# Kernel tuning notes

Hardware: AMD Instinct MI355X
Metric: run time of the kernel (lower is better)

Reference implementation:

```python
import jax, jax.numpy as jnp
import numpy as np

B, S, D, H = 2, 2048, 1024, 16
DH = D // H  # 64


def setup_inputs() -> dict:
    key = jax.random.key(0)
    ks = jax.random.split(key, 9)
    scale = 0.02
    x = jax.random.normal(ks[0], (B, S, D), dtype=jnp.float32)
    # per-head QKV weights stacked over heads: [H, D, DH]
    Wq = jax.random.normal(ks[1], (H, D, DH), dtype=jnp.float32) * scale
    Wk = jax.random.normal(ks[2], (H, D, DH), dtype=jnp.float32) * scale
    Wv = jax.random.normal(ks[3], (H, D, DH), dtype=jnp.float32) * scale
    bq = jax.random.normal(ks[4], (H, DH), dtype=jnp.float32) * scale
    bk = jax.random.normal(ks[5], (H, DH), dtype=jnp.float32) * scale
    bv = jax.random.normal(ks[6], (H, DH), dtype=jnp.float32) * scale
    Wo = jax.random.normal(ks[7], (D, D), dtype=jnp.float32) * scale
    bo = jax.random.normal(ks[8], (D,), dtype=jnp.float32) * scale
    return {"x": x, "Wq": Wq, "bq": bq, "Wk": Wk, "bk": bk, "Wv": Wv, "bv": bv, "Wo": Wo, "bo": bo}


def reference(x, Wq, bq, Wk, bk, Wv, bv, Wo, bo):
    # per-head projections: [B, H, S, DH]
    q = jnp.einsum('bsd,hde->bhse', x, Wq) + bq[None, :, None, :]
    k = jnp.einsum('bsd,hde->bhse', x, Wk) + bk[None, :, None, :]
    v = jnp.einsum('bsd,hde->bhse', x, Wv) + bv[None, :, None, :]
    scores = jnp.einsum('bhse,bhte->bhst', q, k) / jnp.sqrt(jnp.float32(DH))
    probs = jax.nn.softmax(scores, axis=-1)  # [B, H, S, S]
    ctx = jnp.einsum('bhst,bhte->bhse', probs, v)  # [B, H, S, DH]
    # concat heads: [B, S, H*DH]
    ctx = jnp.transpose(ctx, (0, 2, 1, 3)).reshape(x.shape[0], x.shape[1], H * DH)
    out = ctx @ Wo + bo  # output projection; dropout p=0 -> identity
    return out
```

## Files before the change

kernel.cpp:

```cpp
#include <hip/hip_runtime.h>

typedef __attribute__((ext_vector_type(8))) short short8;
typedef __attribute__((ext_vector_type(4))) float f32x4;
typedef __attribute__((ext_vector_type(16))) float f32x16;
typedef __attribute__((ext_vector_type(4))) unsigned short us4;
typedef unsigned short ushort;

typedef __attribute__((address_space(3))) void lds_void;
typedef __attribute__((address_space(1))) void gbl_void;

__device__ __forceinline__ ushort f2bf(float f) {
  unsigned u = __float_as_uint(f);
  u += 0x7fff + ((u >> 16) & 1);
  return (ushort)(u >> 16);
}

__global__ void cvt_x_kernel(const float* __restrict__ x, ushort* __restrict__ xb) {
  int i = (blockIdx.x * 256 + threadIdx.x) * 8;
  float4 a = *(const float4*)(x + i);
  float4 b = *(const float4*)(x + i + 4);
  ushort o[8];
  o[0] = f2bf(a.x); o[1] = f2bf(a.y); o[2] = f2bf(a.z); o[3] = f2bf(a.w);
  o[4] = f2bf(b.x); o[5] = f2bf(b.y); o[6] = f2bf(b.z); o[7] = f2bf(b.w);
  *(short8*)(xb + i) = *(short8*)o;
}

__global__ void wprep_kernel(const float* __restrict__ Wq, const float* __restrict__ Wk,
                             const float* __restrict__ Wv, const float* __restrict__ Wo,
                             ushort* __restrict__ wqkv_t, ushort* __restrict__ wo_t) {
  __shared__ float T[64][65];
  const int k0 = blockIdx.x * 64;
  const int hy = blockIdx.y;
  const int m = blockIdx.z;
  const float* src = (m == 0) ? Wq : (m == 1) ? Wk : (m == 2) ? Wv : Wo;
#pragma unroll
  for (int it = 0; it < 16; ++it) {
    int idx = it * 256 + threadIdx.x;
    int kk = idx >> 6, e = idx & 63;
    float v = (m < 3) ? src[hy * 65536 + (k0 + kk) * 64 + e]
                      : src[(k0 + kk) * 1024 + hy * 64 + e];
    T[e][kk] = v;
  }
  __syncthreads();
  ushort* dst = (m < 3) ? (wqkv_t + (size_t)(m * 1024 + hy * 64) * 1024)
                        : (wo_t + (size_t)(hy * 64) * 1024);
#pragma unroll
  for (int it = 0; it < 2; ++it) {
    int c = it * 256 + threadIdx.x;
    int e = c >> 3, kc = (c & 7) * 8;
    ushort o[8];
#pragma unroll
    for (int j = 0; j < 8; ++j) o[j] = f2bf(T[e][kc + j]);
    *(short8*)&dst[(size_t)e * 1024 + k0 + kc] = *(short8*)o;
  }
}

__global__ __launch_bounds__(512, 2) void gemm_qkv256(
    const ushort* __restrict__ A, const ushort* __restrict__ Bt,
    const float* __restrict__ b0, const float* __restrict__ b1, const float* __restrict__ b2,
    ushort* __restrict__ qfp, ushort* __restrict__ kfp, ushort* __restrict__ vfp) {
  __shared__ ushort sm[3][2][256][32];
  const int tid = threadIdx.x;
  const int lane = tid & 63;
  const int wave = tid >> 6;
  const int l15 = lane & 15, l4 = lane >> 4;
  const int wwr = wave >> 2, wc = wave & 3;
  const int p0 = blockIdx.x;
  const int p = (p0 & 7) * 24 + (p0 >> 3);
  const int by = p & 15, bx = p >> 4;
  const int row0 = by * 256, col0 = bx * 256;

  const ushort* Ag = A + (size_t)row0 * 1024;
  const ushort* Bg = Bt + (size_t)col0 * 1024;
  char* smb = (char*)&sm[0][0][0][0];

  auto stage = [&](int buf, int kt, int c0) {
    const int c = c0 + tid;
    const int row = (c & 1023) >> 2;
    const int slot = c & 3;
    const int scol = (slot ^ ((row >> 1) & 3)) * 8;
    const ushort* src = ((c >> 10) ? Bg : Ag) + (size_t)row * 1024 + kt * 32 + scol;
    __builtin_amdgcn_global_load_lds((const gbl_void*)src,
        (lds_void*)(smb + buf * 32768 + (c0 + (tid & ~63)) * 16), 16, 0, 0);
  };
  auto rdA = [&](int buf, int mfg) {
    const int row = wwr * 128 + mfg * 16 + l15;
    return *(const short8*)(smb + buf * 32768 + row * 64 + ((l4 ^ ((row >> 1) & 3)) << 4));
  };
  auto rdB = [&](int buf, int nf) {
    const int row = wc * 64 + nf * 16 + l15;
    return *(const short8*)(smb + buf * 32768 + 16384 + row * 64 + ((l4 ^ ((row >> 1) & 3)) << 4));
  };

  f32x4 acc[8][4];
#pragma unroll
  for (int i = 0; i < 8; ++i)
#pragma unroll
    for (int j = 0; j < 4; ++j) acc[i][j] = (f32x4){0.f, 0.f, 0.f, 0.f};

  stage(0, 0, 0); stage(0, 0, 512); stage(0, 0, 1024); stage(0, 0, 1536);
  stage(1, 1, 0); stage(1, 1, 512); stage(1, 1, 1024); stage(1, 1, 1536);

  int buf = 0;
  for (int kt = 0; kt < 32; ++kt) {
    if (kt == 31) asm volatile("s_waitcnt vmcnt(0)" ::: "memory");
    else          asm volatile("s_waitcnt vmcnt(4)" ::: "memory");
    asm volatile("s_barrier" ::: "memory");
    const int kn = kt + 2;
    const int bn = (buf >= 1) ? buf - 1 : buf + 2;
    short8 bfr[4], af[4];
#pragma unroll
    for (int nf = 0; nf < 4; ++nf) bfr[nf] = rdB(buf, nf);
#pragma unroll
    for (int mf = 0; mf < 4; ++mf) af[mf] = rdA(buf, mf);
    if (kn < 32) { stage(bn, kn, 0); stage(bn, kn, 512); }
    __builtin_amdgcn_s_setprio(1);
#pragma unroll
    for (int mf = 0; mf < 4; ++mf)
#pragma unroll
      for (int nf = 0; nf < 4; ++nf)
        acc[mf][nf] = __builtin_amdgcn_mfma_f32_16x16x32_bf16(af[mf], bfr[nf], acc[mf][nf], 0, 0, 0);
    __builtin_amdgcn_s_setprio(0);
    asm volatile("s_barrier" ::: "memory");
#pragma unroll
    for (int mf = 0; mf < 4; ++mf) af[mf] = rdA(buf, 4 + mf);
    if (kn < 32) { stage(bn, kn, 1024); stage(bn, kn, 1536); }
    __builtin_amdgcn_s_setprio(1);
#pragma unroll
    for (int mf = 0; mf < 4; ++mf)
#pragma unroll
      for (int nf = 0; nf < 4; ++nf)
        acc[4 + mf][nf] = __builtin_amdgcn_mfma_f32_16x16x32_bf16(af[mf], bfr[nf], acc[4 + mf][nf], 0, 0, 0);
    __builtin_amdgcn_s_setprio(0);
    buf = (buf == 2) ? 0 : buf + 1;
  }

  const float QSCALE = 0.18033688f;
#pragma unroll
  for (int mfg = 0; mfg < 8; ++mfg) {
    const int row = row0 + wwr * 128 + mfg * 16 + l4 * 4;
    const int bb = row >> 11, s = row & 2047;
#pragma unroll
    for (int nf = 0; nf < 4; ++nf) {
      const int col = col0 + wc * 64 + nf * 16 + l15;
      if (col < 2048) {
        const int cf = col & 1023;
        const int h = cf >> 6, d = cf & 63;
        const int bh = bb * 16 + h;
        ushort* dst = (col < 1024) ? qfp : kfp;
        const float bias = ((col < 1024) ? b0 : b1)[cf];
        const float sc = (col < 1024) ? QSCALE : 1.0f;
        const size_t base =
            ((((size_t)bh * 64 + (s >> 5)) * 4 + (d >> 4)) * 64 + ((d >> 3) & 1) * 32 + (s & 31)) * 8 +
            (d & 7);
#pragma unroll
        for (int r = 0; r < 4; ++r) dst[base + r * 8] = f2bf((acc[mfg][nf][r] + bias) * sc);
      } else {
        const int ef = col - 2048;
        const int h = ef >> 6, e = ef & 63;
        const int bh = bb * 16 + h;
        const float bias = b2[ef];
        ushort o4[4];
#pragma unroll
        for (int r = 0; r < 4; ++r) o4[r] = f2bf(acc[mfg][nf][r] + bias);
        const size_t addr =
            ((((size_t)bh * 2 + (e >> 5)) * 128 + (s >> 4)) * 64 + ((s >> 3) & 1) * 32 + (e & 31)) * 8 +
            (s & 7);
        *(us4*)&vfp[addr] = *(us4*)o4;
      }
    }
  }
}

__global__ __launch_bounds__(256) void gemm_out_kernel(
    const ushort* __restrict__ A, const ushort* __restrict__ Bt,
    const float* __restrict__ b0, float* __restrict__ C) {
  __shared__ ushort lA[128 * 32];
  __shared__ ushort lB[128 * 32];
  const int tid = threadIdx.x;
  const int lane = tid & 63;
  const int wave = tid >> 6;
  const int l15 = lane & 15, l4 = lane >> 4;
  const int wr = wave >> 1, wc = wave & 1;
  const int row0 = blockIdx.y * 128, col0 = blockIdx.x * 128;

  f32x4 acc[4][4];
#pragma unroll
  for (int i = 0; i < 4; ++i)
#pragma unroll
    for (int j = 0; j < 4; ++j) acc[i][j] = (f32x4){0.f, 0.f, 0.f, 0.f};

  const ushort* Ag = A + (size_t)row0 * 1024;
  const ushort* Bg = Bt + (size_t)col0 * 1024;

  for (int k0 = 0; k0 < 1024; k0 += 32) {
#pragma unroll
    for (int c = 0; c < 2; ++c) {
      const int chunk = tid + c * 256;
      const int rr = chunk >> 2;
      const int kc = (chunk & 3) * 8;
      const unsigned lbase = (unsigned)((tid & ~63) + c * 256) * 16;
      __builtin_amdgcn_global_load_lds((const gbl_void*)(Ag + (size_t)rr * 1024 + k0 + kc),
                                       (lds_void*)((char*)lA + lbase), 16, 0, 0);
      __builtin_amdgcn_global_load_lds((const gbl_void*)(Bg + (size_t)rr * 1024 + k0 + kc),
                                       (lds_void*)((char*)lB + lbase), 16, 0, 0);
    }
    __syncthreads();
    short8 af[4], bfr[4];
#pragma unroll
    for (int i = 0; i < 4; ++i)
      af[i] = *(const short8*)&lA[(wr * 64 + i * 16 + l15) * 32 + l4 * 8];
#pragma unroll
    for (int j = 0; j < 4; ++j)
      bfr[j] = *(const short8*)&lB[(wc * 64 + j * 16 + l15) * 32 + l4 * 8];
#pragma unroll
    for (int i = 0; i < 4; ++i)
#pragma unroll
      for (int j = 0; j < 4; ++j)
        acc[i][j] = __builtin_amdgcn_mfma_f32_16x16x32_bf16(af[i], bfr[j], acc[i][j], 0, 0, 0);
    __syncthreads();
  }

#pragma unroll
  for (int i = 0; i < 4; ++i) {
    const int row = row0 + wr * 64 + i * 16 + l4 * 4;
#pragma unroll
    for (int j = 0; j < 4; ++j) {
      const int col = col0 + wc * 64 + j * 16 + l15;
      const float bias = b0[col];
#pragma unroll
      for (int r = 0; r < 4; ++r)
        C[(size_t)(row + r) * 1024 + col] = acc[i][j][r] + bias;
    }
  }
}

__global__ __launch_bounds__(256, 2) void attn_kernel(const ushort* __restrict__ qf,
                                                      const ushort* __restrict__ kf,
                                                      const ushort* __restrict__ vf,
                                                      ushort* __restrict__ ctx) {
  __shared__ ushort sm[4][8192];
  const int tid = threadIdx.x;
  const int lane = tid & 63, wave = tid >> 6;
  const int l31 = lane & 31, hi = lane >> 5;
  const int p0 = blockIdx.x;
  const int idx = p0 >> 3;
  const int bh = (p0 & 7) * 4 + (idx >> 4);
  const int q0 = ((idx & 15) * 4 + wave) * 32;
  const int b = bh >> 4, h = bh & 15;

  const size_t bhbase = (size_t)bh * 131072;
  const ushort* qfb = qf + bhbase + (size_t)(q0 >> 5) * 2048 + (size_t)lane * 8;
  const ushort* kfbh = kf + bhbase;
  const ushort* vfbh = vf + bhbase;
  char* smb = (char*)&sm[0][0];

  short8 qb[4];
#pragma unroll
  for (int kk = 0; kk < 4; ++kk)
    qb[kk] = *(const short8*)(qfb + kk * 512);

  auto stage = [&](int buf, int t0) {
    const ushort* s0 = kfbh + (size_t)(t0 >> 5) * 2048 + tid * 8;
    const ushort* s1 = s0 + 2048;
    const ushort* s2 = vfbh + (size_t)(t0 >> 4) * 512 + tid * 8;
    const ushort* s3 = s2 + 65536;
    char* d = smb + buf * 16384 + (tid & ~63) * 16;
    __builtin_amdgcn_global_load_lds((const gbl_void*)s0, (lds_void*)(d), 16, 0, 0);
    __builtin_amdgcn_global_load_lds((const gbl_void*)s1, (lds_void*)(d + 4096), 16, 0, 0);
    __builtin_amdgcn_global_load_lds((const gbl_void*)s2, (lds_void*)(d + 8192), 16, 0, 0);
    __builtin_amdgcn_global_load_lds((const gbl_void*)s3, (lds_void*)(d + 12288), 16, 0, 0);
  };

  f32x16 cacc[2];
#pragma unroll
  for (int me = 0; me < 2; ++me)
#pragma unroll
    for (int r = 0; r < 16; ++r) cacc[me][r] = 0.f;
  float l_run = 0.f;

  stage(0, 0);
  stage(1, 64);
  for (int it = 0; it < 32; ++it) {
    if (it < 31) asm volatile("s_waitcnt vmcnt(4)" ::: "memory");
    else         asm volatile("s_waitcnt vmcnt(0)" ::: "memory");
    asm volatile("s_barrier" ::: "memory");

    const int cur = it & 3;
    const char* kb = smb + cur * 16384;
    const char* vb = kb + 8192;

    short8 ka[2][4], va[2][4];
#pragma unroll
    for (int me = 0; me < 2; ++me)
#pragma unroll
      for (int kk = 0; kk < 4; ++kk)
        ka[me][kk] = *(const short8*)(kb + me * 4096 + kk * 1024 + lane * 16);
#pragma unroll
    for (int mev = 0; mev < 2; ++mev)
#pragma unroll
      for (int kk = 0; kk < 4; ++kk)
        va[mev][kk] = *(const short8*)(vb + mev * 4096 + kk * 1024 + lane * 16);

    if (it < 30) stage((it + 2) & 3, (it + 2) * 64);

    f32x16 sacc[2];
    __builtin_amdgcn_s_setprio(1);
#pragma unroll
    for (int me = 0; me < 2; ++me) {
#pragma unroll
      for (int r = 0; r < 16; ++r) sacc[me][r] = 0.f;
#pragma unroll
      for (int kk = 0; kk < 4; ++kk)
        sacc[me] = __builtin_amdgcn_mfma_f32_32x32x16_bf16(ka[me][kk], qb[kk], sacc[me], 0, 0, 0);
    }
    __builtin_amdgcn_s_setprio(0);

    float s0 = 0.f, s1 = 0.f, s2 = 0.f, s3 = 0.f;
    unsigned w[2][8];
#pragma unroll
    for (int me = 0; me < 2; ++me) {
      float pp[16];
#pragma unroll
      for (int r = 0; r < 16; r += 4) {
        pp[r + 0] = __builtin_amdgcn_exp2f(sacc[me][r + 0]);
        pp[r + 1] = __builtin_amdgcn_exp2f(sacc[me][r + 1]);
        pp[r + 2] = __builtin_amdgcn_exp2f(sacc[me][r + 2]);
        pp[r + 3] = __builtin_amdgcn_exp2f(sacc[me][r + 3]);
        s0 += pp[r + 0]; s1 += pp[r + 1]; s2 += pp[r + 2]; s3 += pp[r + 3];
      }
#pragma unroll
      for (int i = 0; i < 8; ++i)
        asm("v_cvt_pk_bf16_f32 %0, %1, %2" : "=v"(w[me][i]) : "v"(pp[2 * i]), "v"(pp[2 * i + 1]));
    }
    l_run += (s0 + s1) + (s2 + s3);

    unsigned pb[4][4];
#pragma unroll
    for (int me = 0; me < 2; ++me)
#pragma unroll
      for (int c = 0; c < 2; ++c) {
        unsigned a0 = w[me][4 * c + 0], a1 = w[me][4 * c + 1];
        unsigned b0r = w[me][4 * c + 2], b1r = w[me][4 * c + 3];
        asm("v_permlane32_swap_b32 %0, %1" : "+v"(a0), "+v"(b0r));
        asm("v_permlane32_swap_b32 %0, %1" : "+v"(a1), "+v"(b1r));
        const int kk = me * 2 + c;
        pb[kk][0] = a0; pb[kk][1] = a1; pb[kk][2] = b0r; pb[kk][3] = b1r;
      }

    __builtin_amdgcn_s_setprio(1);
#pragma unroll
    for (int mev = 0; mev < 2; ++mev)
#pragma unroll
      for (int kk = 0; kk < 4; ++kk)
        cacc[mev] = __builtin_amdgcn_mfma_f32_32x32x16_bf16(va[mev][kk], *(const short8*)&pb[kk][0],
                                                            cacc[mev], 0, 0, 0);
    __builtin_amdgcn_s_setprio(0);
  }

  l_run += __shfl_xor(l_run, 32);
  const float inv = 1.f / l_run;
  const int q = q0 + l31;
#pragma unroll
  for (int mev = 0; mev < 2; ++mev)
#pragma unroll
    for (int g = 0; g < 4; ++g) {
      ushort o4[4];
#pragma unroll
      for (int rr = 0; rr < 4; ++rr)
        o4[rr] = f2bf(cacc[mev][g * 4 + rr] * inv);
      const int e0 = mev * 32 + 8 * g + 4 * hi;
      *(us4*)&ctx[(size_t)(b * 2048 + q) * 1024 + h * 64 + e0] = *(us4*)o4;
    }
}

extern "C" void kernel_launch(void* const* d_in, const int* in_sizes, int n_in,
                              void* d_out, int out_size, void* d_ws, size_t ws_size,
                              hipStream_t stream) {
  const float* x = (const float*)d_in[0];
  const float* Wq = (const float*)d_in[1];
  const float* bq = (const float*)d_in[2];
  const float* Wk = (const float*)d_in[3];
  const float* bk = (const float*)d_in[4];
  const float* Wv = (const float*)d_in[5];
  const float* bv = (const float*)d_in[6];
  const float* Wo = (const float*)d_in[7];
  const float* bo = (const float*)d_in[8];
  float* out = (float*)d_out;

  char* ws = (char*)d_ws;
  ushort* xb = (ushort*)ws;
  ushort* ctx = xb;
  ushort* wqkv_t = (ushort*)(ws + 8u * 1024 * 1024);
  ushort* wo_t = (ushort*)(ws + 14u * 1024 * 1024);
  ushort* qf = (ushort*)(ws + 16u * 1024 * 1024);
  ushort* kf = (ushort*)(ws + 24u * 1024 * 1024);
  ushort* vf = (ushort*)(ws + 32u * 1024 * 1024);

  cvt_x_kernel<<<dim3(2048), dim3(256), 0, stream>>>(x, xb);
  wprep_kernel<<<dim3(16, 16, 4), dim3(256), 0, stream>>>(Wq, Wk, Wv, Wo, wqkv_t, wo_t);
  gemm_qkv256<<<dim3(192), dim3(512), 0, stream>>>(xb, wqkv_t, bq, bk, bv, qf, kf, vf);
  attn_kernel<<<dim3(512), dim3(256), 0, stream>>>(qf, kf, vf, ctx);
  gemm_out_kernel<<<dim3(8, 32), dim3(256), 0, stream>>>(ctx, wo_t, bo, out);
}
```

Baseline: 118.3 us.

## Software-pipeline QK^T MFMA one tile ahead of softmax and PV

Restructures the attention loop so the QK^T MFMAs for tile it+1 are issued before the exp2/convert/permlane work and PV MFMAs of tile it. Two score accumulators are ping-ponged, and the loop is unrolled by two through a lambda. The aim is to overlap the matrix-core work with the VALU softmax work. This raises register pressure (an extra 32 accumulator VGPRs), which could reduce occupancy or cause spills.

```diff
diff --git a/kernel.cpp b/kernel.cpp
--- a/kernel.cpp
+++ b/kernel.cpp
@@ -279,42 +279,63 @@
     for (int r = 0; r < 16; ++r) cacc[me][r] = 0.f;
   float l_run = 0.f;
 
+  short8 ka[2][4];
+  f32x16 saccA[2], saccB[2];
+
   stage(0, 0);
   stage(1, 64);
-  for (int it = 0; it < 32; ++it) {
-    if (it < 31) asm volatile("s_waitcnt vmcnt(4)" ::: "memory");
-    else         asm volatile("s_waitcnt vmcnt(0)" ::: "memory");
-    asm volatile("s_barrier" ::: "memory");
-
-    const int cur = it & 3;
-    const char* kb = smb + cur * 16384;
-    const char* vb = kb + 8192;
-
-    short8 ka[2][4], va[2][4];
-#pragma unroll
-    for (int me = 0; me < 2; ++me)
-#pragma unroll
-      for (int kk = 0; kk < 4; ++kk)
-        ka[me][kk] = *(const short8*)(kb + me * 4096 + kk * 1024 + lane * 16);
+  asm volatile("s_waitcnt vmcnt(4)" ::: "memory");
+  asm volatile("s_barrier" ::: "memory");
+#pragma unroll
+  for (int me = 0; me < 2; ++me)
+#pragma unroll
+    for (int kk = 0; kk < 4; ++kk)
+      ka[me][kk] = *(const short8*)(smb + me * 4096 + kk * 1024 + lane * 16);
+  stage(2, 128);
+  __builtin_amdgcn_s_setprio(1);
+#pragma unroll
+  for (int me = 0; me < 2; ++me) {
+#pragma unroll
+    for (int r = 0; r < 16; ++r) saccA[me][r] = 0.f;
+#pragma unroll
+    for (int kk = 0; kk < 4; ++kk)
+      saccA[me] = __builtin_amdgcn_mfma_f32_32x32x16_bf16(ka[me][kk], qb[kk], saccA[me], 0, 0, 0);
+  }
+  __builtin_amdgcn_s_setprio(0);
+
+  auto body = [&](f32x16 (&cur)[2], f32x16 (&nxt)[2], int it) {
+    if (it < 31) {
+      if (it < 30) asm volatile("s_waitcnt vmcnt(4)" ::: "memory");
+      else         asm volatile("s_waitcnt vmcnt(0)" ::: "memory");
+      asm volatile("s_barrier" ::: "memory");
+      const char* kbn = smb + ((it + 1) & 3) * 16384;
+#pragma unroll
+      for (int me = 0; me < 2; ++me)
+#pragma unroll
+        for (int kk = 0; kk < 4; ++kk)
+          ka[me][kk] = *(const short8*)(kbn + me * 4096 + kk * 1024 + lane * 16);
+      if (it < 29) stage((it + 3) & 3, (it + 3) * 64);
+    }
+    const char* vb = smb + (it & 3) * 16384 + 8192;
+    short8 va[2][4];
 #pragma unroll
     for (int mev = 0; mev < 2; ++mev)
 #pragma unroll
       for (int kk = 0; kk < 4; ++kk)
         va[mev][kk] = *(const short8*)(vb + mev * 4096 + kk * 1024 + lane * 16);
 
-    if (it < 30) stage((it + 2) & 3, (it + 2) * 64);
-
-    f32x16 sacc[2];
-    __builtin_amdgcn_s_setprio(1);
-#pragma unroll
-    for (int me = 0; me < 2; ++me) {
-#pragma unroll
-      for (int r = 0; r < 16; ++r) sacc[me][r] = 0.f;
-#pragma unroll
-      for (int kk = 0; kk < 4; ++kk)
-        sacc[me] = __builtin_amdgcn_mfma_f32_32x32x16_bf16(ka[me][kk], qb[kk], sacc[me], 0, 0, 0);
-    }
-    __builtin_amdgcn_s_setprio(0);
+    if (it < 31) {
+      __builtin_amdgcn_s_setprio(1);
+#pragma unroll
+      for (int me = 0; me < 2; ++me) {
+#pragma unroll
+        for (int r = 0; r < 16; ++r) nxt[me][r] = 0.f;
+#pragma unroll
+        for (int kk = 0; kk < 4; ++kk)
+          nxt[me] = __builtin_amdgcn_mfma_f32_32x32x16_bf16(ka[me][kk], qb[kk], nxt[me], 0, 0, 0);
+      }
+      __builtin_amdgcn_s_setprio(0);
+    }
 
     float s0 = 0.f, s1 = 0.f, s2 = 0.f, s3 = 0.f;
     unsigned w[2][8];
@@ -323,10 +344,10 @@
       float pp[16];
 #pragma unroll
       for (int r = 0; r < 16; r += 4) {
-        pp[r + 0] = __builtin_amdgcn_exp2f(sacc[me][r + 0]);
-        pp[r + 1] = __builtin_amdgcn_exp2f(sacc[me][r + 1]);
-        pp[r + 2] = __builtin_amdgcn_exp2f(sacc[me][r + 2]);
-        pp[r + 3] = __builtin_amdgcn_exp2f(sacc[me][r + 3]);
+        pp[r + 0] = __builtin_amdgcn_exp2f(cur[me][r + 0]);
+        pp[r + 1] = __builtin_amdgcn_exp2f(cur[me][r + 1]);
+        pp[r + 2] = __builtin_amdgcn_exp2f(cur[me][r + 2]);
+        pp[r + 3] = __builtin_amdgcn_exp2f(cur[me][r + 3]);
         s0 += pp[r + 0]; s1 += pp[r + 1]; s2 += pp[r + 2]; s3 += pp[r + 3];
       }
 #pragma unroll
@@ -356,6 +377,11 @@
         cacc[mev] = __builtin_amdgcn_mfma_f32_32x32x16_bf16(va[mev][kk], *(const short8*)&pb[kk][0],
                                                             cacc[mev], 0, 0, 0);
     __builtin_amdgcn_s_setprio(0);
+  };
+
+  for (int itp = 0; itp < 32; itp += 2) {
+    body(saccA, saccB, itp);
+    body(saccB, saccA, itp + 1);
   }
 
   l_run += __shfl_xor(l_run, 32);
```

After: 119.4 us. Within noise of the previous version (+1.0%).

## Split attention key range across two wave groups per block and merge in LDS

Applied to the files above, without the earlier changes.

The attention block grows from 4 to 8 waves. Each group of 4 waves processes half of the key/value sequence for the same 128 queries with its own double-buffered LDS staging. Partial context accumulators and row sums are then combined through shared memory before normalization and the bf16 store. This doubles wave-level parallelism and shortens each wave's serial key loop, meant to hide latency better. The cost is a shallower prefetch pipeline (two buffers with a full vmcnt wait each iteration), an extra LDS reduction step, and a much tighter register budget from the new launch bounds, which risks spills.

```diff
diff --git a/kernel.cpp b/kernel.cpp
--- a/kernel.cpp
+++ b/kernel.cpp
@@ -235,25 +235,27 @@
   }
 }
 
-__global__ __launch_bounds__(256, 2) void attn_kernel(const ushort* __restrict__ qf,
+__global__ __launch_bounds__(512, 4) void attn_kernel(const ushort* __restrict__ qf,
                                                       const ushort* __restrict__ kf,
                                                       const ushort* __restrict__ vf,
                                                       ushort* __restrict__ ctx) {
-  __shared__ ushort sm[4][8192];
+  __shared__ ushort sm[2][2][8192];
   const int tid = threadIdx.x;
   const int lane = tid & 63, wave = tid >> 6;
+  const int grp = wave >> 2, gw = wave & 3;
+  const int gtid = tid & 255;
   const int l31 = lane & 31, hi = lane >> 5;
   const int p0 = blockIdx.x;
   const int idx = p0 >> 3;
   const int bh = (p0 & 7) * 4 + (idx >> 4);
-  const int q0 = ((idx & 15) * 4 + wave) * 32;
+  const int q0 = ((idx & 15) * 4 + gw) * 32;
   const int b = bh >> 4, h = bh & 15;
 
   const size_t bhbase = (size_t)bh * 131072;
   const ushort* qfb = qf + bhbase + (size_t)(q0 >> 5) * 2048 + (size_t)lane * 8;
   const ushort* kfbh = kf + bhbase;
   const ushort* vfbh = vf + bhbase;
-  char* smb = (char*)&sm[0][0];
+  char* gsm = (char*)&sm[grp][0][0];
 
   short8 qb[4];
 #pragma unroll
@@ -261,11 +263,11 @@
     qb[kk] = *(const short8*)(qfb + kk * 512);
 
   auto stage = [&](int buf, int t0) {
-    const ushort* s0 = kfbh + (size_t)(t0 >> 5) * 2048 + tid * 8;
+    const ushort* s0 = kfbh + (size_t)(t0 >> 5) * 2048 + gtid * 8;
     const ushort* s1 = s0 + 2048;
-    const ushort* s2 = vfbh + (size_t)(t0 >> 4) * 512 + tid * 8;
+    const ushort* s2 = vfbh + (size_t)(t0 >> 4) * 512 + gtid * 8;
     const ushort* s3 = s2 + 65536;
-    char* d = smb + buf * 16384 + (tid & ~63) * 16;
+    char* d = gsm + buf * 16384 + (gtid & ~63) * 16;
     __builtin_amdgcn_global_load_lds((const gbl_void*)s0, (lds_void*)(d), 16, 0, 0);
     __builtin_amdgcn_global_load_lds((const gbl_void*)s1, (lds_void*)(d + 4096), 16, 0, 0);
     __builtin_amdgcn_global_load_lds((const gbl_void*)s2, (lds_void*)(d + 8192), 16, 0, 0);
@@ -279,15 +281,14 @@
     for (int r = 0; r < 16; ++r) cacc[me][r] = 0.f;
   float l_run = 0.f;
 
-  stage(0, 0);
-  stage(1, 64);
-  for (int it = 0; it < 32; ++it) {
-    if (it < 31) asm volatile("s_waitcnt vmcnt(4)" ::: "memory");
-    else         asm volatile("s_waitcnt vmcnt(0)" ::: "memory");
+  const int tbase = grp * 1024;
+  stage(0, tbase);
+  for (int it = 0; it < 16; ++it) {
+    asm volatile("s_waitcnt vmcnt(0)" ::: "memory");
     asm volatile("s_barrier" ::: "memory");
-
-    const int cur = it & 3;
-    const char* kb = smb + cur * 16384;
+    if (it < 15) stage((it + 1) & 1, tbase + (it + 1) * 64);
+
+    const char* kb = gsm + (it & 1) * 16384;
     const char* vb = kb + 8192;
 
     short8 ka[2][4], va[2][4];
@@ -301,8 +302,6 @@
 #pragma unroll
       for (int kk = 0; kk < 4; ++kk)
         va[mev][kk] = *(const short8*)(vb + mev * 4096 + kk * 1024 + lane * 16);
-
-    if (it < 30) stage((it + 2) & 3, (it + 2) * 64);
 
     f32x16 sacc[2];
     __builtin_amdgcn_s_setprio(1);
@@ -359,19 +358,36 @@
   }
 
   l_run += __shfl_xor(l_run, 32);
-  const float inv = 1.f / l_run;
-  const int q = q0 + l31;
-#pragma unroll
-  for (int mev = 0; mev < 2; ++mev)
-#pragma unroll
-    for (int g = 0; g < 4; ++g) {
-      ushort o4[4];
-#pragma unroll
-      for (int rr = 0; rr < 4; ++rr)
-        o4[rr] = f2bf(cacc[mev][g * 4 + rr] * inv);
-      const int e0 = mev * 32 + 8 * g + 4 * hi;
-      *(us4*)&ctx[(size_t)(b * 2048 + q) * 1024 + h * 64 + e0] = *(us4*)o4;
-    }
+  __syncthreads();
+  float* mb = (float*)&sm[0][0][0];
+  if (grp == 1) {
+#pragma unroll
+    for (int mev = 0; mev < 2; ++mev)
+#pragma unroll
+      for (int r = 0; r < 16; ++r)
+        mb[(mev * 16 + r) * 256 + gw * 64 + lane] = cacc[mev][r];
+    mb[8192 + gw * 64 + lane] = l_run;
+  }
+  __syncthreads();
+  if (grp == 0) {
+    const float l1 = mb[8192 + gw * 64 + lane];
+    const float inv = 1.f / (l_run + l1);
+    const int q = q0 + l31;
+#pragma unroll
+    for (int mev = 0; mev < 2; ++mev)
+#pragma unroll
+      for (int g = 0; g < 4; ++g) {
+        ushort o4[4];
+#pragma unroll
+        for (int rr = 0; rr < 4; ++rr) {
+          const int r = g * 4 + rr;
+          const float v = (cacc[mev][r] + mb[(mev * 16 + r) * 256 + gw * 64 + lane]) * inv;
+          o4[rr] = f2bf(v);
+        }
+        const int e0 = mev * 32 + 8 * g + 4 * hi;
+        *(us4*)&ctx[(size_t)(b * 2048 + q) * 1024 + h * 64 + e0] = *(us4*)o4;
+      }
+  }
 }
 
 extern "C" void kernel_launch(void* const* d_in, const int* in_sizes, int n_in,
@@ -400,6 +416,6 @@
   cvt_x_kernel<<<dim3(2048), dim3(256), 0, stream>>>(x, xb);
   wprep_kernel<<<dim3(16, 16, 4), dim3(256), 0, stream>>>(Wq, Wk, Wv, Wo, wqkv_t, wo_t);
   gemm_qkv256<<<dim3(192), dim3(512), 0, stream>>>(xb, wqkv_t, bq, bk, bv, qf, kf, vf);
-  attn_kernel<<<dim3(512), dim3(256), 0, stream>>>(qf, kf, vf, ctx);
+  attn_kernel<<<dim3(512), dim3(512), 0, stream>>>(qf, kf, vf, ctx);
   gemm_out_kernel<<<dim3(8, 32), dim3(256), 0, stream>>>(ctx, wo_t, bo, out);
 }
```

Result: slower. 131.4 us (+11.1%).
